# Optimization experiments

Measured on AMD Instinct MI355X. Metric: run time of the kernel, lower is better.

## Reference

```python
import jax, jax.numpy as jnp
import numpy as np

BATCH, SEQ, IN_DIM = 4, 2048, 4
D_MODEL, HEADS, D_HEAD = 128, 8, 16
DEPTH, BUCKET, N_HASHES = 6, 64, 8
D_FF = 4 * D_MODEL
NUM_CLASSES = 2
NB = SEQ // BUCKET          # 32 buckets per hash round
SELF_ATTN_VALUE = -5e4      # lucidrains TOKEN_SELF_ATTN_VALUE


def setup_inputs() -> dict:
    key = jax.random.key(0)
    ks = jax.random.split(key, 12)
    rn = lambda k, s: jax.random.normal(k, s, jnp.float32) * 0.02
    return {
        "x": jax.random.normal(ks[0], (BATCH, SEQ, IN_DIM), jnp.float32),
        "emb_W": rn(ks[1], (IN_DIM, D_MODEL)),
        "emb_b": jnp.zeros((D_MODEL,), jnp.float32),
        "Wqk": rn(ks[2], (DEPTH, D_MODEL, D_MODEL)),
        "Wv": rn(ks[3], (DEPTH, D_MODEL, D_MODEL)),
        "Wo": rn(ks[4], (DEPTH, D_MODEL, D_MODEL)),
        "R": jax.random.normal(ks[5], (DEPTH, HEADS, D_HEAD, N_HASHES, NB // 2), jnp.float32),
        "ln1_g": jnp.ones((DEPTH, D_MODEL), jnp.float32),
        "ln1_b": jnp.zeros((DEPTH, D_MODEL), jnp.float32),
        "ln2_g": jnp.ones((DEPTH, D_MODEL), jnp.float32),
        "ln2_b": jnp.zeros((DEPTH, D_MODEL), jnp.float32),
        "ff_W1": rn(ks[6], (DEPTH, D_MODEL, D_FF)),
        "ff_b1": jnp.zeros((DEPTH, D_FF), jnp.float32),
        "ff_W2": rn(ks[7], (DEPTH, D_FF, D_MODEL)),
        "ff_b2": jnp.zeros((DEPTH, D_MODEL), jnp.float32),
        "fc_W": rn(ks[8], (D_MODEL, NUM_CLASSES)),
        "fc_b": jnp.zeros((NUM_CLASSES,), jnp.float32),
    }


def layer_norm(x, g, b, eps=1e-5):
    m = x.mean(-1, keepdims=True)
    v = ((x - m) ** 2).mean(-1, keepdims=True)
    return (x - m) * jax.lax.rsqrt(v + eps) * g + b


def lsh_attention(x, wqk, wv, wo, rot):
    # x: [B,S,D]; rot: [H, dh, n_hashes, NB//2]. Shared-QK LSH attention (eval mode, no dropout).
    B, S, D = x.shape
    qk = (x @ wqk).reshape(B, S, HEADS, D_HEAD).transpose(0, 2, 1, 3)  # [B,H,S,dh]
    v = (x @ wv).reshape(B, S, HEADS, D_HEAD).transpose(0, 2, 1, 3)

    # --- hashing: argmax over [xR; -xR] rotations ---
    rx = jnp.einsum('bhsd,hdnr->bhnsr', qk, rot)                # [B,H,n_hashes,S,NB/2]
    buckets = jnp.argmax(jnp.concatenate([rx, -rx], -1), -1)    # [B,H,n_hashes,S] in [0,NB)
    buckets = buckets + (jnp.arange(N_HASHES) * NB)[None, None, :, None]
    buckets = buckets.reshape(B, HEADS, N_HASHES * S)

    # --- stable sort by (bucket, position) ---
    ticker = jnp.arange(N_HASHES * S)
    sticker = jnp.argsort(buckets * S + (ticker % S), axis=-1)   # [B,H,L]
    undo = jnp.argsort(sticker, axis=-1)
    st = sticker % S                                              # original positions

    sqk = jnp.take_along_axis(qk, st[..., None], axis=2)          # [B,H,L,dh]
    sv = jnp.take_along_axis(v, st[..., None], axis=2)

    n_chunks = N_HASHES * NB
    bq = sqk.reshape(B, HEADS, n_chunks, BUCKET, D_HEAD)
    bk = bq / jnp.linalg.norm(bq, axis=-1, keepdims=True)         # shared-QK: keys are normalized queries
    bv = sv.reshape(B, HEADS, n_chunks, BUCKET, D_HEAD)
    bt = st.reshape(B, HEADS, n_chunks, BUCKET)

    look_back = lambda t: jnp.concatenate([t, jnp.roll(t, 1, axis=2)], axis=3)
    bk, bv, bkt = look_back(bk), look_back(bv), look_back(bt)

    dots = jnp.einsum('bhcid,bhcjd->bhcij', bq, bk) * (D_HEAD ** -0.5)  # [B,H,C,64,128]
    dots = jnp.where(bt[..., :, None] == bkt[..., None, :], SELF_ATTN_VALUE, dots)

    logsum = jax.nn.logsumexp(dots, axis=-1)                      # [B,H,C,64]
    probs = jnp.exp(dots - logsum[..., None])
    bo = jnp.einsum('bhcij,bhcjd->bhcid', probs, bv)

    so = bo.reshape(B, HEADS, N_HASHES * S, D_HEAD)
    slog = logsum.reshape(B, HEADS, N_HASHES * S)
    o = jnp.take_along_axis(so, undo[..., None], axis=2).reshape(B, HEADS, N_HASHES, S, D_HEAD)
    logits = jnp.take_along_axis(slog, undo, axis=2).reshape(B, HEADS, N_HASHES, S, 1)

    w = jax.nn.softmax(logits, axis=2)                            # combine hash rounds
    out = (o * w).sum(axis=2)                                     # [B,H,S,dh]
    out = out.transpose(0, 2, 1, 3).reshape(B, S, D)
    return out @ wo


def reference(x, emb_W, emb_b, Wqk, Wv, Wo, R, ln1_g, ln1_b, ln2_g, ln2_b,
              ff_W1, ff_b1, ff_W2, ff_b2, fc_W, fc_b):
    h = x @ emb_W + emb_b

    def layer(h, p):
        wqk, wv, wo, r, g1, b1g, g2, b2g, w1, bb1, w2, bb2 = p
        h = h + lsh_attention(layer_norm(h, g1, b1g), wqk, wv, wo, r)
        y = layer_norm(h, g2, b2g)
        h = h + (jax.nn.gelu(y @ w1 + bb1) @ w2 + bb2)
        return h, None

    h, _ = jax.lax.scan(layer, h, (Wqk, Wv, Wo, R, ln1_g, ln1_b, ln2_g, ln2_b,
                                   ff_W1, ff_b1, ff_W2, ff_b2))
    return h.mean(axis=1) @ fc_W + fc_b
```

## Files before the change

kernel.cpp:

```cpp
#include <hip/hip_runtime.h>
#include <math.h>

#define BB 4
#define SS 2048
#define INDIM 4
#define DD 128
#define HH 8
#define DH 16
#define DEPTH 6
#define BUCKET 64
#define NHASH 8
#define NBK 32
#define DFF 512
#define LL (NHASH*SS)
#define NCHUNK (NHASH*NBK)
#define NBH (BB*HH)

typedef short bf16x8 __attribute__((ext_vector_type(8)));
typedef _Float16 f16x8 __attribute__((ext_vector_type(8)));
typedef float f32x4 __attribute__((ext_vector_type(4)));

__device__ __forceinline__ unsigned short f2bf(float f) {
    unsigned u = __builtin_bit_cast(unsigned, f);
    unsigned r = u + 0x7FFFu + ((u >> 16) & 1u);
    return (unsigned short)(r >> 16);
}

__global__ void k_embed(const float* __restrict__ x, const float* __restrict__ W,
                        const float* __restrict__ b, float* __restrict__ h) {
    int idx = blockIdx.x * blockDim.x + threadIdx.x;
    if (idx >= BB*SS*DD) return;
    int d = idx % DD, bs = idx / DD;
    const float* xr = x + bs*INDIM;
    float acc = b[d];
    #pragma unroll
    for (int k = 0; k < INDIM; k++) acc += xr[k] * W[k*DD + d];
    h[idx] = acc;
}

__global__ void k_wcast(const float* __restrict__ src, unsigned short* __restrict__ dst,
                        int R, int C) {
    __shared__ float tile[32][33];
    int l = blockIdx.z;
    const float* s = src + (size_t)l*R*C;
    unsigned short* d = dst + (size_t)l*R*C;
    int c0 = blockIdx.x*32, r0 = blockIdx.y*32;
    int tx = threadIdx.x, ty = threadIdx.y;
    #pragma unroll
    for (int i = 0; i < 4; i++)
        tile[ty + i*8][tx] = s[(size_t)(r0 + ty + i*8)*C + c0 + tx];
    __syncthreads();
    #pragma unroll
    for (int i = 0; i < 4; i++)
        d[(size_t)(c0 + ty + i*8)*R + r0 + tx] = f2bf(tile[tx][ty + i*8]);
}

__global__ void k_wcast16(const float* __restrict__ src, _Float16* __restrict__ dst,
                          int R, int C) {
    __shared__ float tile[32][33];
    int l = blockIdx.z;
    const float* s = src + (size_t)l*R*C;
    _Float16* d = dst + (size_t)l*R*C;
    int c0 = blockIdx.x*32, r0 = blockIdx.y*32;
    int tx = threadIdx.x, ty = threadIdx.y;
    #pragma unroll
    for (int i = 0; i < 4; i++)
        tile[ty + i*8][tx] = s[(size_t)(r0 + ty + i*8)*C + c0 + tx];
    __syncthreads();
    #pragma unroll
    for (int i = 0; i < 4; i++)
        d[(size_t)(c0 + ty + i*8)*R + r0 + tx] = (_Float16)tile[tx][ty + i*8];
}

__global__ __launch_bounds__(256, 4)
void k_proj_qkv(const float* __restrict__ hin, const float* __restrict__ lng,
                const float* __restrict__ lnb, const _Float16* __restrict__ WqkT,
                const _Float16* __restrict__ WvT, float* __restrict__ qk,
                float* __restrict__ v) {
    __shared__ float A[16][128];
    __shared__ __align__(16) _Float16 Lf[16][136];
    int row0 = blockIdx.x * 16;
    int t = threadIdx.x;
    {
        const float4* src = (const float4*)(hin + (size_t)row0*DD);
        float4* dst = (float4*)&A[0][0];
        dst[t]       = src[t];
        dst[t + 256] = src[t + 256];
    }
    __syncthreads();
    {
        int r = t >> 4, sub = t & 15;
        float4 xa = *(const float4*)&A[r][sub*8];
        float4 xb = *(const float4*)&A[r][sub*8 + 4];
        float s = xa.x+xa.y+xa.z+xa.w + xb.x+xb.y+xb.z+xb.w;
        s += __shfl_xor(s,1); s += __shfl_xor(s,2);
        s += __shfl_xor(s,4); s += __shfl_xor(s,8);
        float m = s * (1.0f/128.0f);
        float d0=xa.x-m, d1=xa.y-m, d2=xa.z-m, d3=xa.w-m;
        float d4=xb.x-m, d5=xb.y-m, d6=xb.z-m, d7=xb.w-m;
        float vs = d0*d0+d1*d1+d2*d2+d3*d3+d4*d4+d5*d5+d6*d6+d7*d7;
        vs += __shfl_xor(vs,1); vs += __shfl_xor(vs,2);
        vs += __shfl_xor(vs,4); vs += __shfl_xor(vs,8);
        float inv = 1.0f / sqrtf(vs * (1.0f/128.0f) + 1e-5f);
        float4 ga = *(const float4*)&lng[sub*8], gb = *(const float4*)&lng[sub*8+4];
        float4 ba = *(const float4*)&lnb[sub*8], bb = *(const float4*)&lnb[sub*8+4];
        f16x8 vv;
        vv[0] = (_Float16)(d0*inv*ga.x + ba.x);
        vv[1] = (_Float16)(d1*inv*ga.y + ba.y);
        vv[2] = (_Float16)(d2*inv*ga.z + ba.z);
        vv[3] = (_Float16)(d3*inv*ga.w + ba.w);
        vv[4] = (_Float16)(d4*inv*gb.x + bb.x);
        vv[5] = (_Float16)(d5*inv*gb.y + bb.y);
        vv[6] = (_Float16)(d6*inv*gb.z + bb.z);
        vv[7] = (_Float16)(d7*inv*gb.w + bb.w);
        *(f16x8*)&Lf[r][sub*8] = vv;
    }
    __syncthreads();
    int w = t >> 6, lane = t & 63;
    int fr = lane & 15, kg = lane >> 4;
    f32x4 aq[2], av[2];
    aq[0] = (f32x4){0.f,0.f,0.f,0.f}; aq[1] = (f32x4){0.f,0.f,0.f,0.f};
    av[0] = (f32x4){0.f,0.f,0.f,0.f}; av[1] = (f32x4){0.f,0.f,0.f,0.f};
    #pragma unroll
    for (int ks = 0; ks < 4; ks++) {
        f16x8 af = *(const f16x8*)&Lf[fr][ks*32 + kg*8];
        #pragma unroll
        for (int nt = 0; nt < 2; nt++) {
            const _Float16* bp = WqkT + (size_t)(w*32 + nt*16 + fr)*128 + ks*32 + kg*8;
            f16x8 bq = *(const f16x8*)bp;
            aq[nt] = __builtin_amdgcn_mfma_f32_16x16x32_f16(af, bq, aq[nt], 0, 0, 0);
            const _Float16* vp = WvT + (size_t)(w*32 + nt*16 + fr)*128 + ks*32 + kg*8;
            f16x8 bv = *(const f16x8*)vp;
            av[nt] = __builtin_amdgcn_mfma_f32_16x16x32_f16(af, bv, av[nt], 0, 0, 0);
        }
    }
    int b = row0 / SS;
    int sb = row0 & (SS-1);
    #pragma unroll
    for (int nt = 0; nt < 2; nt++) {
        int n = w*32 + nt*16 + fr;
        int h_ = n >> 4, d_ = n & 15;
        #pragma unroll
        for (int i = 0; i < 4; i++) {
            int s = sb + kg*4 + i;
            size_t o = (((size_t)(b*HH + h_))*SS + s)*DH + d_;
            qk[o] = aq[nt][i]; v[o] = av[nt][i];
        }
    }
}

__global__ void k_hash(const float* __restrict__ qk, const float* __restrict__ R,
                       int* __restrict__ bkt) {
    __shared__ float Rs[256];
    int idx = blockIdx.x*256 + threadIdx.x;
    int s = idx & (SS-1); int t2 = idx >> 11;
    int n = t2 & 7; int bh = t2 >> 3; int h_ = bh & 7;
    {
        int tt = threadIdx.x;
        int d = tt >> 4, r = tt & 15;
        Rs[tt] = R[(((h_*DH + d)*NHASH + n)*16) + r];
    }
    __syncthreads();
    const float4* q4 = (const float4*)(qk + ((size_t)bh*SS + s)*DH);
    float4 q0 = q4[0], q1 = q4[1], q2 = q4[2], q3 = q4[3];
    float rxv[16];
    #pragma unroll
    for (int r = 0; r < 16; r++) {
        rxv[r] = q0.x*Rs[  0+r] + q0.y*Rs[ 16+r] + q0.z*Rs[ 32+r] + q0.w*Rs[ 48+r]
               + q1.x*Rs[ 64+r] + q1.y*Rs[ 80+r] + q1.z*Rs[ 96+r] + q1.w*Rs[112+r]
               + q2.x*Rs[128+r] + q2.y*Rs[144+r] + q2.z*Rs[160+r] + q2.w*Rs[176+r]
               + q3.x*Rs[192+r] + q3.y*Rs[208+r] + q3.z*Rs[224+r] + q3.w*Rs[240+r];
    }
    float best = rxv[0]; int bi = 0;
    #pragma unroll
    for (int jx = 1; jx < 16; jx++) if (rxv[jx]  > best) { best = rxv[jx];  bi = jx; }
    #pragma unroll
    for (int jx = 0; jx < 16; jx++) if (-rxv[jx] > best) { best = -rxv[jx]; bi = 16 + jx; }
    bkt[idx] = n*NBK + bi;
}

__global__ void k_scatter(const int* __restrict__ bkt, int* __restrict__ sticker) {
    __shared__ int hist[256*33];
    __shared__ int cs[8*33];
    __shared__ int bbk[NBK];
    int blk = blockIdx.x;
    int n = blk & 7, bh = blk >> 3;
    int t = threadIdx.x;
    #pragma unroll
    for (int k = 0; k < NBK; k++) hist[t*33 + k] = 0;
    const int* bp = bkt + (size_t)bh*LL + n*SS;
    int local[8];
    #pragma unroll
    for (int e = 0; e < 8; e++) {
        int k = bp[t*8 + e] - n*NBK;
        local[e] = k;
        hist[t*33 + k]++;
    }
    __syncthreads();
    {
        int i = t >> 5, k = t & 31;
        int ssum = 0;
        #pragma unroll
        for (int rr = 0; rr < 32; rr++) ssum += hist[(i*32+rr)*33 + k];
        cs[i*33 + k] = ssum;
    }
    __syncthreads();
    if (t < 32) {
        int tot = 0;
        #pragma unroll
        for (int i = 0; i < 8; i++) tot += cs[i*33 + t];
        int x = tot;
        #pragma unroll
        for (int o = 1; o < 32; o <<= 1) {
            int y = __shfl(x, (t >= o) ? (t - o) : 0, 64);
            if (t >= o) x += y;
        }
        bbk[t] = n*SS + x - tot;
    }
    __syncthreads();
    {
        int i = t >> 5, k = t & 31;
        int run = bbk[k];
        for (int ii = 0; ii < i; ii++) run += cs[ii*33 + k];
        for (int rr = 0; rr < 32; rr++) {
            int idx = (i*32+rr)*33 + k;
            int c0 = hist[idx];
            hist[idx] = run;
            run += c0;
        }
    }
    __syncthreads();
    #pragma unroll
    for (int e = 0; e < 8; e++) {
        int k = local[e];
        int pos = hist[t*33 + k]++;
        sticker[(size_t)bh*LL + pos] = n*SS + t*8 + e;
    }
}

__global__ __launch_bounds__(256, 4)
void k_attn(const float* __restrict__ qk, const float* __restrict__ v,
            const int* __restrict__ sticker, _Float16* __restrict__ so,
            float* __restrict__ slog) {
    __shared__ __align__(16) char smem[33024];
    _Float16 (*Kf)[40]  = (_Float16(*)[40])smem;
    _Float16 (*P)[136]  = (_Float16(*)[136])(smem + 10240);
    _Float16 (*VT)[136] = (_Float16(*)[136])(smem + 27648);
    int*   pk   = (int*)(smem + 32000);
    float* nrm  = (float*)(smem + 32512);
    int*   lraw = (int*)(smem + 32768);

    int blk = blockIdx.x;
    int c = blk & (NCHUNK-1), bh = blk >> 8;
    int t = threadIdx.x;
    const int* stk = sticker + (size_t)bh*LL;
    const float4* qkb = (const float4*)(qk + (size_t)bh*SS*DH);
    const float4* vb  = (const float4*)(v  + (size_t)bh*SS*DH);

    if (t < 128) {
        int j = t;
        int cc = (j < 64) ? c : ((c + NCHUNK - 1) & (NCHUNK-1));
        int raw = stk[cc*BUCKET + (j & 63)];
        int sk = raw & (SS-1);
        float4 k0 = qkb[sk*4+0], k1 = qkb[sk*4+1], k2 = qkb[sk*4+2], k3 = qkb[sk*4+3];
        float ssq = k0.x*k0.x + k0.y*k0.y + k0.z*k0.z + k0.w*k0.w
                  + k1.x*k1.x + k1.y*k1.y + k1.z*k1.z + k1.w*k1.w
                  + k2.x*k2.x + k2.y*k2.y + k2.z*k2.z + k2.w*k2.w
                  + k3.x*k3.x + k3.y*k3.y + k3.z*k3.z + k3.w*k3.w;
        float nn = sqrtf(ssq);
        float inv = 1.0f / nn;
        f16x8 z = {0,0,0,0,0,0,0,0};
        f16x8 kf0, kf1;
        kf0[0]=(_Float16)(k0.x*inv); kf0[1]=(_Float16)(k0.y*inv);
        kf0[2]=(_Float16)(k0.z*inv); kf0[3]=(_Float16)(k0.w*inv);
        kf0[4]=(_Float16)(k1.x*inv); kf0[5]=(_Float16)(k1.y*inv);
        kf0[6]=(_Float16)(k1.z*inv); kf0[7]=(_Float16)(k1.w*inv);
        kf1[0]=(_Float16)(k2.x*inv); kf1[1]=(_Float16)(k2.y*inv);
        kf1[2]=(_Float16)(k2.z*inv); kf1[3]=(_Float16)(k2.w*inv);
        kf1[4]=(_Float16)(k3.x*inv); kf1[5]=(_Float16)(k3.y*inv);
        kf1[6]=(_Float16)(k3.z*inv); kf1[7]=(_Float16)(k3.w*inv);
        *(f16x8*)&Kf[j][0]  = kf0; *(f16x8*)&Kf[j][8]  = kf1;
        *(f16x8*)&Kf[j][16] = z;   *(f16x8*)&Kf[j][24] = z;
        pk[j] = sk;
        if (j < 64) { nrm[j] = nn * 0.25f; lraw[j] = raw; }
    } else {
        int j = t - 128;
        int cc = (j < 64) ? c : ((c + NCHUNK - 1) & (NCHUNK-1));
        int sk = stk[cc*BUCKET + (j & 63)] & (SS-1);
        float4 v0 = vb[sk*4+0], v1 = vb[sk*4+1], v2 = vb[sk*4+2], v3 = vb[sk*4+3];
        VT[ 0][j]=(_Float16)v0.x; VT[ 1][j]=(_Float16)v0.y;
        VT[ 2][j]=(_Float16)v0.z; VT[ 3][j]=(_Float16)v0.w;
        VT[ 4][j]=(_Float16)v1.x; VT[ 5][j]=(_Float16)v1.y;
        VT[ 6][j]=(_Float16)v1.z; VT[ 7][j]=(_Float16)v1.w;
        VT[ 8][j]=(_Float16)v2.x; VT[ 9][j]=(_Float16)v2.y;
        VT[10][j]=(_Float16)v2.z; VT[11][j]=(_Float16)v2.w;
        VT[12][j]=(_Float16)v3.x; VT[13][j]=(_Float16)v3.y;
        VT[14][j]=(_Float16)v3.z; VT[15][j]=(_Float16)v3.w;
    }
    __syncthreads();

    int w = t >> 6, lane = t & 63;
    int fr = lane & 15, kg = lane >> 4;
    int qrow = w*16 + fr;

    f32x4 acc[8];
    #pragma unroll
    for (int nt = 0; nt < 8; nt++) acc[nt] = (f32x4){0.f,0.f,0.f,0.f};
    {
        f16x8 kfq = *(const f16x8*)&Kf[qrow][kg*8];
        _Float16 qs = (_Float16)nrm[qrow];
        f16x8 a0 = kfq * qs;
        #pragma unroll
        for (int nt = 0; nt < 8; nt++) {
            f16x8 bfr = *(const f16x8*)&Kf[nt*16 + fr][kg*8];
            acc[nt] = __builtin_amdgcn_mfma_f32_16x16x32_f16(a0, bfr, acc[nt], 0, 0, 0);
        }
    }
    int pq[4], lr[4];
    #pragma unroll
    for (int i = 0; i < 4; i++) {
        int r = w*16 + kg*4 + i;
        pq[i] = pk[r]; lr[i] = lraw[r];
    }
    float s[4] = {0.f, 0.f, 0.f, 0.f};
    #pragma unroll
    for (int nt = 0; nt < 8; nt++) {
        int pkk = pk[nt*16 + fr];
        #pragma unroll
        for (int i = 0; i < 4; i++) {
            float d = acc[nt][i];
            d = (pq[i] == pkk) ? -5e4f : d;
            float p = __expf(d);
            s[i] += p;
            P[w*16 + kg*4 + i][nt*16 + fr] = (_Float16)p;
        }
    }
    #pragma unroll
    for (int i = 0; i < 4; i++) {
        s[i] += __shfl_xor(s[i], 1); s[i] += __shfl_xor(s[i], 2);
        s[i] += __shfl_xor(s[i], 4); s[i] += __shfl_xor(s[i], 8);
    }

    f32x4 oacc = (f32x4){0.f,0.f,0.f,0.f};
    #pragma unroll
    for (int ks = 0; ks < 4; ks++) {
        f16x8 af = *(const f16x8*)&P[w*16 + fr][ks*32 + kg*8];
        f16x8 bf = *(const f16x8*)&VT[fr][ks*32 + kg*8];
        oacc = __builtin_amdgcn_mfma_f32_16x16x32_f16(af, bf, oacc, 0, 0, 0);
    }
    #pragma unroll
    for (int i = 0; i < 4; i++) {
        float invs = 1.0f / s[i];
        int l = lr[i];
        so[((size_t)bh*LL + l)*DH + fr] = (_Float16)(oacc[i] * invs);
        if (fr == 0) slog[(size_t)bh*LL + l] = __logf(s[i]);
    }
}

__global__ __launch_bounds__(256, 2)
void k_out_ffn(const _Float16* __restrict__ so, const float* __restrict__ slog,
               const _Float16* __restrict__ WoT, const float* __restrict__ lng,
               const float* __restrict__ lnb, const unsigned short* __restrict__ W1T,
               const float* __restrict__ b1, const unsigned short* __restrict__ W2T,
               const float* __restrict__ b2, float* __restrict__ h) {
    __shared__ float hs[16][128];
    __shared__ __align__(16) _Float16 At[16][136];
    __shared__ __align__(16) unsigned short Albf[16][136];
    __shared__ __align__(16) unsigned short albf[16][520];
    int row0 = blockIdx.x * 16;
    int t = threadIdx.x;
    int b = row0 / SS;
    int s0 = row0 & (SS-1);

    {
        const float4* src = (const float4*)(h + (size_t)row0*DD);
        float4* dst = (float4*)&hs[0][0];
        dst[t]       = src[t];
        dst[t + 256] = src[t + 256];
    }
    {
        int half = t & 1, task = t >> 1;
        int r = task >> 3, h_ = task & 7;
        int s = s0 + r;
        int bh = b*HH + h_;
        const float* sl = slog + (size_t)bh*LL + s;
        float lg[NHASH];
        float m = -3.4e38f;
        #pragma unroll
        for (int n = 0; n < NHASH; n++) {
            lg[n] = sl[n*SS];
            m = fmaxf(m, lg[n]);
        }
        float sum = 0.f;
        #pragma unroll
        for (int n = 0; n < NHASH; n++) { lg[n] = __expf(lg[n] - m); sum += lg[n]; }
        float inv = 1.0f / sum;
        float o[8] = {0,0,0,0,0,0,0,0};
        #pragma unroll
        for (int n = 0; n < NHASH; n++) {
            float wgt = lg[n]*inv;
            const f16x8* sp = (const f16x8*)(so + ((size_t)bh*LL + n*SS + s)*DH + half*8);
            f16x8 a = *sp;
            #pragma unroll
            for (int j = 0; j < 8; j++) o[j] += wgt*(float)a[j];
        }
        f16x8 ov;
        #pragma unroll
        for (int j = 0; j < 8; j++) ov[j] = (_Float16)o[j];
        *(f16x8*)&At[r][h_*16 + half*8] = ov;
    }
    __syncthreads();

    int w = t >> 6, lane = t & 63;
    int fr = lane & 15, kg = lane >> 4;

    {
        f32x4 ao[2];
        ao[0] = (f32x4){0.f,0.f,0.f,0.f}; ao[1] = (f32x4){0.f,0.f,0.f,0.f};
        #pragma unroll
        for (int ks = 0; ks < 4; ks++) {
            f16x8 af = *(const f16x8*)&At[fr][ks*32 + kg*8];
            #pragma unroll
            for (int nt = 0; nt < 2; nt++) {
                const _Float16* bp = WoT + (size_t)(w*32 + nt*16 + fr)*128 + ks*32 + kg*8;
                f16x8 bf = *(const f16x8*)bp;
                ao[nt] = __builtin_amdgcn_mfma_f32_16x16x32_f16(af, bf, ao[nt], 0, 0, 0);
            }
        }
        #pragma unroll
        for (int nt = 0; nt < 2; nt++)
            #pragma unroll
            for (int i = 0; i < 4; i++)
                hs[kg*4 + i][w*32 + nt*16 + fr] += ao[nt][i];
    }
    __syncthreads();

    {
        int r = t >> 4, sub = t & 15;
        float4 xa = *(const float4*)&hs[r][sub*8];
        float4 xb = *(const float4*)&hs[r][sub*8 + 4];
        float s = xa.x+xa.y+xa.z+xa.w + xb.x+xb.y+xb.z+xb.w;
        s += __shfl_xor(s,1); s += __shfl_xor(s,2);
        s += __shfl_xor(s,4); s += __shfl_xor(s,8);
        float m = s * (1.0f/128.0f);
        float d0=xa.x-m, d1=xa.y-m, d2=xa.z-m, d3=xa.w-m;
        float d4=xb.x-m, d5=xb.y-m, d6=xb.z-m, d7=xb.w-m;
        float vs = d0*d0+d1*d1+d2*d2+d3*d3+d4*d4+d5*d5+d6*d6+d7*d7;
        vs += __shfl_xor(vs,1); vs += __shfl_xor(vs,2);
        vs += __shfl_xor(vs,4); vs += __shfl_xor(vs,8);
        float inv = 1.0f / sqrtf(vs * (1.0f/128.0f) + 1e-5f);
        float4 ga = *(const float4*)&lng[sub*8], gb = *(const float4*)&lng[sub*8+4];
        float4 ba = *(const float4*)&lnb[sub*8], bb = *(const float4*)&lnb[sub*8+4];
        bf16x8 vv;
        vv[0] = (short)f2bf(d0*inv*ga.x + ba.x);
        vv[1] = (short)f2bf(d1*inv*ga.y + ba.y);
        vv[2] = (short)f2bf(d2*inv*ga.z + ba.z);
        vv[3] = (short)f2bf(d3*inv*ga.w + ba.w);
        vv[4] = (short)f2bf(d4*inv*gb.x + bb.x);
        vv[5] = (short)f2bf(d5*inv*gb.y + bb.y);
        vv[6] = (short)f2bf(d6*inv*gb.z + bb.z);
        vv[7] = (short)f2bf(d7*inv*gb.w + bb.w);
        *(bf16x8*)&Albf[r][sub*8] = vv;
    }
    __syncthreads();

    f32x4 acc1[8];
    #pragma unroll
    for (int i = 0; i < 8; i++) acc1[i] = (f32x4){0.f, 0.f, 0.f, 0.f};
    {
        const unsigned short* w1p = W1T + (size_t)(w*128 + fr)*128 + kg*8;
        #pragma unroll
        for (int ks = 0; ks < 4; ks++) {
            bf16x8 af = *(const bf16x8*)&Albf[fr][ks*32 + kg*8];
            #pragma unroll
            for (int nt = 0; nt < 8; nt++) {
                bf16x8 bf = *(const bf16x8*)(w1p + nt*16*128 + ks*32);
                acc1[nt] = __builtin_amdgcn_mfma_f32_16x16x32_bf16(af, bf, acc1[nt], 0, 0, 0);
            }
        }
    }
    #pragma unroll
    for (int nt = 0; nt < 8; nt++) {
        int col = w*128 + nt*16 + fr;
        float bias = b1[col];
        #pragma unroll
        for (int i = 0; i < 4; i++) {
            int row = kg*4 + i;
            float x = acc1[nt][i] + bias;
            float t0 = tanhf(0.7978845608028654f * (x + 0.044715f*x*x*x));
            albf[row][col] = f2bf(0.5f*x*(1.0f + t0));
        }
    }
    __syncthreads();

    f32x4 acc2[2];
    acc2[0] = (f32x4){0.f,0.f,0.f,0.f};
    acc2[1] = (f32x4){0.f,0.f,0.f,0.f};
    {
        const unsigned short* w2p = W2T + (size_t)(w*32 + fr)*512 + kg*8;
        #pragma unroll
        for (int ks = 0; ks < 16; ks++) {
            bf16x8 af = *(const bf16x8*)&albf[fr][ks*32 + kg*8];
            bf16x8 b0 = *(const bf16x8*)(w2p + ks*32);
            bf16x8 b1f = *(const bf16x8*)(w2p + 16*512 + ks*32);
            acc2[0] = __builtin_amdgcn_mfma_f32_16x16x32_bf16(af, b0, acc2[0], 0, 0, 0);
            acc2[1] = __builtin_amdgcn_mfma_f32_16x16x32_bf16(af, b1f, acc2[1], 0, 0, 0);
        }
    }
    #pragma unroll
    for (int nt = 0; nt < 2; nt++) {
        int col = w*32 + nt*16 + fr;
        float bias = b2[col];
        #pragma unroll
        for (int i = 0; i < 4; i++) {
            int row = kg*4 + i;
            h[(size_t)(row0 + row)*DD + col] = hs[row][col] + acc2[nt][i] + bias;
        }
    }
}

__global__ void k_pool(const float* __restrict__ h, float* __restrict__ partial) {
    int blk = blockIdx.x;
    int t = threadIdx.x;
    int b = blk >> 6, c = blk & 63;
    const float* hp = h + ((size_t)b*SS + c*32)*DD + t;
    float acc = 0.f;
    #pragma unroll
    for (int i = 0; i < 32; i++) acc += hp[i*DD];
    partial[blk*DD + t] = acc;
}

__global__ void k_final(const float* __restrict__ partial, const float* __restrict__ fcW,
                        const float* __restrict__ fcb, float* __restrict__ out) {
    __shared__ float red[4];
    int b = blockIdx.x, t = threadIdx.x;
    const float* pp = partial + (size_t)b*64*DD + t;
    float acc = 0.f;
    #pragma unroll
    for (int c = 0; c < 64; c++) acc += pp[c*DD];
    float pooled = acc * (1.0f/(float)SS);
    float p0 = pooled * fcW[t*2+0];
    float p1 = pooled * fcW[t*2+1];
    #pragma unroll
    for (int o = 32; o >= 1; o >>= 1) { p0 += __shfl_xor(p0,o); p1 += __shfl_xor(p1,o); }
    int w = t >> 6;
    if ((t & 63) == 0) { red[w*2] = p0; red[w*2+1] = p1; }
    __syncthreads();
    if (t == 0) {
        out[b*2 + 0] = red[0] + red[2] + fcb[0];
        out[b*2 + 1] = red[1] + red[3] + fcb[1];
    }
}

extern "C" void kernel_launch(void* const* d_in, const int* in_sizes, int n_in,
                              void* d_out, int out_size, void* d_ws, size_t ws_size,
                              hipStream_t stream) {
    const float* x    = (const float*)d_in[0];
    const float* embW = (const float*)d_in[1];
    const float* embB = (const float*)d_in[2];
    const float* Wqk  = (const float*)d_in[3];
    const float* Wv   = (const float*)d_in[4];
    const float* Wo   = (const float*)d_in[5];
    const float* R    = (const float*)d_in[6];
    const float* ln1g = (const float*)d_in[7];
    const float* ln1b = (const float*)d_in[8];
    const float* ln2g = (const float*)d_in[9];
    const float* ln2b = (const float*)d_in[10];
    const float* W1   = (const float*)d_in[11];
    const float* b1   = (const float*)d_in[12];
    const float* W2   = (const float*)d_in[13];
    const float* b2   = (const float*)d_in[14];
    const float* fcW  = (const float*)d_in[15];
    const float* fcb  = (const float*)d_in[16];
    float* out = (float*)d_out;

    char* w = (char*)d_ws;
    auto carve = [&](size_t bytes) -> char* {
        char* p = w;
        w += (bytes + 255) & ~(size_t)255;
        return p;
    };
    float* h       = (float*)carve((size_t)BB*SS*DD*4);
    float* qk      = (float*)carve((size_t)NBH*SS*DH*4);
    float* v       = (float*)carve((size_t)NBH*SS*DH*4);
    int*   bkt     = (int*)  carve((size_t)NBH*LL*4);
    int*   sticker = (int*)  carve((size_t)NBH*LL*4);
    _Float16* so   = (_Float16*)carve((size_t)NBH*LL*DH*2);
    float* slog    = (float*)carve((size_t)NBH*LL*4);
    float* partial = (float*)carve((size_t)BB*64*DD*4);
    unsigned short* w1t = (unsigned short*)carve((size_t)DEPTH*DD*DFF*2);
    unsigned short* w2t = (unsigned short*)carve((size_t)DEPTH*DFF*DD*2);
    _Float16* wqk16 = (_Float16*)carve((size_t)DEPTH*DD*DD*2);
    _Float16* wv16  = (_Float16*)carve((size_t)DEPTH*DD*DD*2);
    _Float16* wo16  = (_Float16*)carve((size_t)DEPTH*DD*DD*2);

    k_wcast<<<dim3(DFF/32, DD/32, DEPTH), dim3(32, 8), 0, stream>>>(W1, w1t, DD, DFF);
    k_wcast<<<dim3(DD/32, DFF/32, DEPTH), dim3(32, 8), 0, stream>>>(W2, w2t, DFF, DD);
    k_wcast16<<<dim3(DD/32, DD/32, DEPTH), dim3(32, 8), 0, stream>>>(Wqk, wqk16, DD, DD);
    k_wcast16<<<dim3(DD/32, DD/32, DEPTH), dim3(32, 8), 0, stream>>>(Wv, wv16, DD, DD);
    k_wcast16<<<dim3(DD/32, DD/32, DEPTH), dim3(32, 8), 0, stream>>>(Wo, wo16, DD, DD);

    k_embed<<<(BB*SS*DD)/256, 256, 0, stream>>>(x, embW, embB, h);

    for (int l = 0; l < DEPTH; l++) {
        const _Float16* wqkl = wqk16 + (size_t)l*DD*DD;
        const _Float16* wvl  = wv16  + (size_t)l*DD*DD;
        const _Float16* wol  = wo16  + (size_t)l*DD*DD;
        const float* rl  = R   + (size_t)l*HH*DH*NHASH*16;
        const float* g1  = ln1g + l*DD; const float* bg1 = ln1b + l*DD;
        const float* g2  = ln2g + l*DD; const float* bg2 = ln2b + l*DD;
        const unsigned short* w1l = w1t + (size_t)l*DD*DFF;
        const unsigned short* w2l = w2t + (size_t)l*DFF*DD;
        const float* bb1 = b1 + l*DFF;
        const float* bb2 = b2 + l*DD;

        k_proj_qkv<<<(BB*SS)/16, 256, 0, stream>>>(h, g1, bg1, wqkl, wvl, qk, v);
        k_hash<<<(NBH*NHASH*SS)/256, 256, 0, stream>>>(qk, rl, bkt);
        k_scatter<<<NBH*NHASH, 256, 0, stream>>>(bkt, sticker);
        k_attn<<<NBH*NCHUNK, 256, 0, stream>>>(qk, v, sticker, so, slog);
        k_out_ffn<<<(BB*SS)/16, 256, 0, stream>>>(so, slog, wol, g2, bg2,
                                                  w1l, bb1, w2l, bb2, h);
    }

    k_pool<<<BB*64, 128, 0, stream>>>(h, partial);
    k_final<<<BB, 128, 0, stream>>>(partial, fcW, fcb, out);
}
```

Before: 551.2 us.

## Transpose QK MFMA, use exp2, defer softmax normalization to hash combine

The QK MFMA operands are swapped so each lane holds one query row. Its row sum then needs only two cross-lane shuffles, and probabilities go out as packed f16x2 stores. Scores are prescaled by log2(e) so exp2f replaces expf. The per-row 1/s normalization is dropped from the attention output, and the hash-round combine uses unnormalized sums scaled by exp(-m)/S. This relies on w_n = s_n*exp(-m)/S, which holds as long as the unnormalized f16 outputs stay in range. Launch bounds of the output/FFN kernel rise to three blocks per SM, which limits registers.

Result: faster. 522.8 us (-5.2%).

```diff
diff --git a/kernel.cpp b/kernel.cpp
--- a/kernel.cpp
+++ b/kernel.cpp
@@ -18,6 +18,7 @@
 
 typedef short bf16x8 __attribute__((ext_vector_type(8)));
 typedef _Float16 f16x8 __attribute__((ext_vector_type(8)));
+typedef _Float16 f16x2 __attribute__((ext_vector_type(2)));
 typedef float f32x4 __attribute__((ext_vector_type(4)));
 
 __device__ __forceinline__ unsigned short f2bf(float f) {
@@ -282,7 +283,7 @@
         *(f16x8*)&Kf[j][0]  = kf0; *(f16x8*)&Kf[j][8]  = kf1;
         *(f16x8*)&Kf[j][16] = z;   *(f16x8*)&Kf[j][24] = z;
         pk[j] = sk;
-        if (j < 64) { nrm[j] = nn * 0.25f; lraw[j] = raw; }
+        if (j < 64) { nrm[j] = nn * 0.25f * 1.4426950408889634f; lraw[j] = raw; }
     } else {
         int j = t - 128;
         int cc = (j < 64) ? c : ((c + NCHUNK - 1) & (NCHUNK-1));
@@ -309,37 +310,32 @@
     {
         f16x8 kfq = *(const f16x8*)&Kf[qrow][kg*8];
         _Float16 qs = (_Float16)nrm[qrow];
-        f16x8 a0 = kfq * qs;
+        f16x8 bq = kfq * qs;
         #pragma unroll
         for (int nt = 0; nt < 8; nt++) {
-            f16x8 bfr = *(const f16x8*)&Kf[nt*16 + fr][kg*8];
-            acc[nt] = __builtin_amdgcn_mfma_f32_16x16x32_f16(a0, bfr, acc[nt], 0, 0, 0);
-        }
-    }
-    int pq[4], lr[4];
-    #pragma unroll
-    for (int i = 0; i < 4; i++) {
-        int r = w*16 + kg*4 + i;
-        pq[i] = pk[r]; lr[i] = lraw[r];
-    }
-    float s[4] = {0.f, 0.f, 0.f, 0.f};
+            f16x8 afk = *(const f16x8*)&Kf[nt*16 + fr][kg*8];
+            acc[nt] = __builtin_amdgcn_mfma_f32_16x16x32_f16(afk, bq, acc[nt], 0, 0, 0);
+        }
+    }
+    int pq_self = pk[qrow];
+    float s = 0.f;
     #pragma unroll
     for (int nt = 0; nt < 8; nt++) {
-        int pkk = pk[nt*16 + fr];
-        #pragma unroll
-        for (int i = 0; i < 4; i++) {
-            float d = acc[nt][i];
-            d = (pq[i] == pkk) ? -5e4f : d;
-            float p = __expf(d);
-            s[i] += p;
-            P[w*16 + kg*4 + i][nt*16 + fr] = (_Float16)p;
-        }
-    }
-    #pragma unroll
-    for (int i = 0; i < 4; i++) {
-        s[i] += __shfl_xor(s[i], 1); s[i] += __shfl_xor(s[i], 2);
-        s[i] += __shfl_xor(s[i], 4); s[i] += __shfl_xor(s[i], 8);
-    }
+        int4 pk4 = *(const int4*)&pk[nt*16 + kg*4];
+        float d0 = (pk4.x == pq_self) ? -5e4f : acc[nt][0];
+        float d1 = (pk4.y == pq_self) ? -5e4f : acc[nt][1];
+        float d2 = (pk4.z == pq_self) ? -5e4f : acc[nt][2];
+        float d3 = (pk4.w == pq_self) ? -5e4f : acc[nt][3];
+        float p0 = exp2f(d0), p1 = exp2f(d1), p2 = exp2f(d2), p3 = exp2f(d3);
+        s += (p0 + p1) + (p2 + p3);
+        f16x2 w0 = {(_Float16)p0, (_Float16)p1};
+        f16x2 w1 = {(_Float16)p2, (_Float16)p3};
+        *(f16x2*)&P[qrow][nt*16 + kg*4]     = w0;
+        *(f16x2*)&P[qrow][nt*16 + kg*4 + 2] = w1;
+    }
+    s += __shfl_xor(s, 16);
+    s += __shfl_xor(s, 32);
+    if (kg == 0) slog[(size_t)bh*LL + lraw[qrow]] = __logf(s);
 
     f32x4 oacc = (f32x4){0.f,0.f,0.f,0.f};
     #pragma unroll
@@ -348,16 +344,16 @@
         f16x8 bf = *(const f16x8*)&VT[fr][ks*32 + kg*8];
         oacc = __builtin_amdgcn_mfma_f32_16x16x32_f16(af, bf, oacc, 0, 0, 0);
     }
-    #pragma unroll
-    for (int i = 0; i < 4; i++) {
-        float invs = 1.0f / s[i];
-        int l = lr[i];
-        so[((size_t)bh*LL + l)*DH + fr] = (_Float16)(oacc[i] * invs);
-        if (fr == 0) slog[(size_t)bh*LL + l] = __logf(s[i]);
-    }
-}
-
-__global__ __launch_bounds__(256, 2)
+    {
+        int4 lr4 = *(const int4*)&lraw[w*16 + kg*4];
+        so[((size_t)bh*LL + lr4.x)*DH + fr] = (_Float16)oacc[0];
+        so[((size_t)bh*LL + lr4.y)*DH + fr] = (_Float16)oacc[1];
+        so[((size_t)bh*LL + lr4.z)*DH + fr] = (_Float16)oacc[2];
+        so[((size_t)bh*LL + lr4.w)*DH + fr] = (_Float16)oacc[3];
+    }
+}
+
+__global__ __launch_bounds__(256, 3)
 void k_out_ffn(const _Float16* __restrict__ so, const float* __restrict__ slog,
                const _Float16* __restrict__ WoT, const float* __restrict__ lng,
                const float* __restrict__ lnb, const unsigned short* __restrict__ W1T,
@@ -391,22 +387,21 @@
             lg[n] = sl[n*SS];
             m = fmaxf(m, lg[n]);
         }
-        float sum = 0.f;
-        #pragma unroll
-        for (int n = 0; n < NHASH; n++) { lg[n] = __expf(lg[n] - m); sum += lg[n]; }
-        float inv = 1.0f / sum;
+        float S = 0.f;
+        #pragma unroll
+        for (int n = 0; n < NHASH; n++) S += __expf(lg[n] - m);
+        float scale = __expf(-m) / S;
         float o[8] = {0,0,0,0,0,0,0,0};
         #pragma unroll
         for (int n = 0; n < NHASH; n++) {
-            float wgt = lg[n]*inv;
             const f16x8* sp = (const f16x8*)(so + ((size_t)bh*LL + n*SS + s)*DH + half*8);
             f16x8 a = *sp;
             #pragma unroll
-            for (int j = 0; j < 8; j++) o[j] += wgt*(float)a[j];
+            for (int j = 0; j < 8; j++) o[j] += (float)a[j];
         }
         f16x8 ov;
         #pragma unroll
-        for (int j = 0; j < 8; j++) ov[j] = (_Float16)o[j];
+        for (int j = 0; j < 8; j++) ov[j] = (_Float16)(o[j] * scale);
         *(f16x8*)&At[r][h_*16 + half*8] = ov;
     }
     __syncthreads();
```
